# Optimization experiments

Hardware: AMD Instinct MI355X
Metric: run time of the kernel (lower is better)

The kernel has to match this reference:

```python
import jax, jax.numpy as jnp
import numpy as np

EMBED = 1024  # point_net_embedding_dim
H1, H2 = 512, 256  # head_hidden_layer_sizes


def _init(key, shape, fan_in):
    return jax.random.normal(key, shape, dtype=jnp.float32) / jnp.sqrt(jnp.float32(fan_in))


def setup_inputs() -> dict:
    key = jax.random.key(0)
    ks = jax.random.split(key, 13)
    B, N = 256, 1024
    x = jax.random.normal(ks[0], (B, N, 3), dtype=jnp.float32)
    # PointNet shared per-point MLP: 3 -> 64 -> 128 -> EMBED (ReLU), max-pool over points
    W1 = _init(ks[1], (3, 64), 3);        b1 = jnp.zeros((64,), jnp.float32)
    W2 = _init(ks[2], (64, 128), 64);     b2 = jnp.zeros((128,), jnp.float32)
    W3 = _init(ks[3], (128, EMBED), 128); b3 = jnp.zeros((EMBED,), jnp.float32)
    # Head MLP: EMBED -> 512 -> 256 -> 9 (no final activation)
    Wh1 = _init(ks[4], (EMBED, H1), EMBED); bh1 = jnp.zeros((H1,), jnp.float32)
    Wh2 = _init(ks[5], (H1, H2), H1);       bh2 = jnp.zeros((H2,), jnp.float32)
    Wh3 = _init(ks[6], (H2, 9), H2);        bh3 = jnp.zeros((9,), jnp.float32)
    return {"x": x, "W1": W1, "b1": b1, "W2": W2, "b2": b2, "W3": W3, "b3": b3,
            "Wh1": Wh1, "bh1": bh1, "Wh2": Wh2, "bh2": bh2, "Wh3": Wh3, "bh3": bh3}


def svd_projection(M):
    # Project raw 3x3 matrices onto SO(3): R = U diag(1,1,det(U V^T)) V^T
    U, S, Vh = jnp.linalg.svd(M, full_matrices=False)
    det = jnp.linalg.det(jnp.einsum('...ij,...jk->...ik', U, Vh))
    d = jnp.stack([jnp.ones_like(det), jnp.ones_like(det), det], axis=-1)  # [..., 3]
    return jnp.einsum('...ij,...j,...jk->...ik', U, d, Vh)


def reference(x, W1, b1, W2, b2, W3, b3, Wh1, bh1, Wh2, bh2, Wh3, bh3):
    # Shared per-point MLP (ReLU), final_activation=ReLU, then max-pool over points
    h = jax.nn.relu(x @ W1 + b1)          # [B, N, 64]
    h = jax.nn.relu(h @ W2 + b2)          # [B, N, 128]
    h = jax.nn.relu(h @ W3 + b3)          # [B, N, EMBED]
    g = jnp.max(h, axis=-2)               # [B, EMBED] global feature
    # Head MLP -> raw 3x3
    z = jax.nn.relu(g @ Wh1 + bh1)
    z = jax.nn.relu(z @ Wh2 + bh2)
    raw = (z @ Wh3 + bh3).reshape(*x.shape[:-2], 3, 3)
    return svd_projection(raw)
```

## Files before the change

### kernel.cpp

```cpp
#include <hip/hip_runtime.h>
#include <math.h>

typedef _Float16 f16;
typedef _Float16 f16x8 __attribute__((ext_vector_type(8)));
typedef float f32x4 __attribute__((ext_vector_type(4)));

__device__ __forceinline__ void glds16(const void* g, void* l) {
    __builtin_amdgcn_global_load_lds(
        (const __attribute__((address_space(1))) unsigned int*)g,
        (__attribute__((address_space(3))) unsigned int*)l, 16, 0, 0);
}

__global__ __launch_bounds__(256, 2) void pointnet_l12(
    const float* __restrict__ x,
    const float* __restrict__ W1, const float* __restrict__ b1,
    const float* __restrict__ W2, const float* __restrict__ b2,
    f16* __restrict__ h2)
{
    __shared__ float xs[512*3];
    __shared__ float w1s[192], b1s[64], b2s[128];
    __shared__ __align__(16) f16 h2s[128*136];

    int tid = threadIdx.x;
    int P0 = blockIdx.x * 512;
    for (int i = tid; i < 1536; i += 256) xs[i] = x[(size_t)P0*3 + i];
    if (tid < 192) w1s[tid] = W1[tid];
    else b1s[tid - 192] = b1[tid - 192];
    if (tid < 128) b2s[tid] = b2[tid];

    int lane = tid & 63, wid = tid >> 6;
    int wr = wid & 1, wc = wid >> 1;
    int lrow = lane & 15, quad = lane >> 4;

    f16x8 bf[4][2];
#pragma unroll
    for (int ct = 0; ct < 4; ct++)
#pragma unroll
        for (int kc = 0; kc < 2; kc++) {
            int col = wc*64 + ct*16 + lrow;
#pragma unroll
            for (int j = 0; j < 8; j++)
                bf[ct][kc][j] = (f16)W2[(size_t)(kc*32 + quad*8 + j)*128 + col];
        }

    __syncthreads();

    for (int mt = 0; mt < 4; mt++) {
        f32x4 acc[4][4];
#pragma unroll
        for (int rt = 0; rt < 4; rt++)
#pragma unroll
            for (int ct = 0; ct < 4; ct++)
                acc[rt][ct] = (f32x4){0.f, 0.f, 0.f, 0.f};

#pragma unroll
        for (int kc = 0; kc < 2; kc++) {
            float wa[8], wb[8], wcv[8], bv[8];
#pragma unroll
            for (int j = 0; j < 8; j++) {
                int k = kc*32 + quad*8 + j;
                wa[j] = w1s[k]; wb[j] = w1s[64+k]; wcv[j] = w1s[128+k]; bv[j] = b1s[k];
            }
            f16x8 af[4];
#pragma unroll
            for (int rt = 0; rt < 4; rt++) {
                int p = mt*128 + wr*64 + rt*16 + lrow;
                float x0 = xs[p*3], x1 = xs[p*3+1], x2 = xs[p*3+2];
#pragma unroll
                for (int j = 0; j < 8; j++) {
                    float v = fmaf(x2, wcv[j], fmaf(x1, wb[j], fmaf(x0, wa[j], bv[j])));
                    af[rt][j] = (f16)fmaxf(v, 0.f);
                }
            }
#pragma unroll
            for (int rt = 0; rt < 4; rt++)
#pragma unroll
                for (int ct = 0; ct < 4; ct++)
                    acc[rt][ct] = __builtin_amdgcn_mfma_f32_16x16x32_f16(af[rt], bf[ct][kc], acc[rt][ct], 0, 0, 0);
        }

        __syncthreads();
#pragma unroll
        for (int rt = 0; rt < 4; rt++)
#pragma unroll
            for (int ct = 0; ct < 4; ct++) {
                int col  = wc*64 + ct*16 + lrow;
                float bb = b2s[col];
                int rowb = wr*64 + rt*16 + quad*4;
#pragma unroll
                for (int r = 0; r < 4; r++) {
                    float v = fmaxf(acc[rt][ct][r] + bb, 0.f);
                    h2s[(rowb + r)*136 + col] = (f16)v;
                }
            }
        __syncthreads();
        size_t gbase = ((size_t)P0 + (size_t)mt*128) * 128;
#pragma unroll
        for (int i = 0; i < 8; i++) {
            int e = i*256 + tid;
            int row = e >> 4, c = e & 15;
            f16x8 v = *(const f16x8*)(h2s + row*136 + c*8);
            *(f16x8*)(h2 + gbase + (size_t)row*128 + ((c ^ (row & 15)) * 8)) = v;
        }
    }
}

__global__ __launch_bounds__(256, 2) void pointnet_l3_max(
    const f16* __restrict__ h2,
    const float* __restrict__ W3,
    const float* __restrict__ b3,
    float* __restrict__ g)
{
    __shared__ __align__(16) f16 atile[2][128 * 128];

    int i  = blockIdx.x;
    int b  = i & 255, nb = i >> 8;
    int tid = threadIdx.x;
    int lane = tid & 63, wid = tid >> 6;
    int lrow = lane & 15, quad = lane >> 4;
    int col0 = nb*256 + wid*64;

    f16x8 bf[4][4];
#pragma unroll
    for (int ct = 0; ct < 4; ct++)
#pragma unroll
        for (int kc = 0; kc < 4; kc++) {
            int col = col0 + ct*16 + lrow;
#pragma unroll
            for (int j = 0; j < 8; j++)
                bf[ct][kc][j] = (f16)W3[(size_t)(kc*32 + quad*8 + j)*1024 + col];
        }

    float cmax[4] = {-3.0e38f, -3.0e38f, -3.0e38f, -3.0e38f};
    const f16* abase = h2 + (size_t)b * 1024 * 128;

    {
        const f16* gsrc = abase;
#pragma unroll
        for (int s = 0; s < 8; s++)
            glds16(gsrc + (wid*512 + s*64 + lane)*8, atile[0] + (wid*512 + s*64)*8);
    }

    int cur = 0;
    for (int m0 = 0; m0 < 1024; m0 += 128) {
        __syncthreads();
        if (m0 + 128 < 1024) {
            const f16* gsrc = abase + (size_t)(m0 + 128) * 128;
            f16* ldst = atile[cur ^ 1];
#pragma unroll
            for (int s = 0; s < 8; s++)
                glds16(gsrc + (wid*512 + s*64 + lane)*8, ldst + (wid*512 + s*64)*8);
        }

        const f16* at = atile[cur];
#pragma unroll
        for (int half = 0; half < 2; half++) {
            f32x4 acc[4][4];
#pragma unroll
            for (int rt = 0; rt < 4; rt++)
#pragma unroll
                for (int ct = 0; ct < 4; ct++)
                    acc[rt][ct] = (f32x4){0.f, 0.f, 0.f, 0.f};
#pragma unroll
            for (int kc = 0; kc < 4; kc++) {
                f16x8 af[4];
#pragma unroll
                for (int rt = 0; rt < 4; rt++) {
                    int row  = half*64 + rt*16 + lrow;
                    int slot = (kc*4 + quad) ^ lrow;
                    af[rt] = *(const f16x8*)(at + row*128 + slot*8);
                }
#pragma unroll
                for (int rt = 0; rt < 4; rt++)
#pragma unroll
                    for (int ct = 0; ct < 4; ct++)
                        acc[rt][ct] = __builtin_amdgcn_mfma_f32_16x16x32_f16(af[rt], bf[ct][kc], acc[rt][ct], 0, 0, 0);
            }
#pragma unroll
            for (int rt = 0; rt < 4; rt++)
#pragma unroll
                for (int ct = 0; ct < 4; ct++)
#pragma unroll
                    for (int r = 0; r < 4; r++)
                        cmax[ct] = fmaxf(cmax[ct], acc[rt][ct][r]);
        }
        cur ^= 1;
    }

#pragma unroll
    for (int ct = 0; ct < 4; ct++) {
        cmax[ct] = fmaxf(cmax[ct], __shfl_xor(cmax[ct], 16, 64));
        cmax[ct] = fmaxf(cmax[ct], __shfl_xor(cmax[ct], 32, 64));
    }
    if (quad == 0) {
#pragma unroll
        for (int ct = 0; ct < 4; ct++) {
            int cg = col0 + ct*16 + lrow;
            g[(size_t)b*1024 + cg] = fmaxf(cmax[ct] + b3[cg], 0.f);
        }
    }
}

__global__ __launch_bounds__(256) void head_l1(
    const float* __restrict__ g, const float* __restrict__ Wh1,
    float* __restrict__ zp1)
{
    __shared__ float gs4[4][256];
    int cb = blockIdx.x, bb = blockIdx.y, kc = blockIdx.z;
    int tid = threadIdx.x;
    int b0 = bb * 4;
    int kbase = kc * 256;
#pragma unroll
    for (int j = 0; j < 4; j++) {
        int i = tid + j*256;
        gs4[i >> 8][i & 255] = g[(size_t)(b0 + (i >> 8))*1024 + kbase + (i & 255)];
    }
    __syncthreads();

    int c = cb*256 + tid;
    float acc[4] = {0.f, 0.f, 0.f, 0.f};
#pragma unroll 1
    for (int k = 0; k < 256; k += 8) {
        float w[8];
#pragma unroll
        for (int j = 0; j < 8; j++) w[j] = Wh1[(size_t)(kbase+k+j)*512 + c];
#pragma unroll
        for (int r = 0; r < 4; r++) {
            float4 a = *(const float4*)&gs4[r][k];
            float4 bq = *(const float4*)&gs4[r][k+4];
            acc[r] = fmaf(a.x, w[0], acc[r]);
            acc[r] = fmaf(a.y, w[1], acc[r]);
            acc[r] = fmaf(a.z, w[2], acc[r]);
            acc[r] = fmaf(a.w, w[3], acc[r]);
            acc[r] = fmaf(bq.x, w[4], acc[r]);
            acc[r] = fmaf(bq.y, w[5], acc[r]);
            acc[r] = fmaf(bq.z, w[6], acc[r]);
            acc[r] = fmaf(bq.w, w[7], acc[r]);
        }
    }
#pragma unroll
    for (int r = 0; r < 4; r++)
        zp1[((size_t)kc*256 + b0 + r)*512 + c] = acc[r];
}

__global__ __launch_bounds__(256) void head_l2(
    const float* __restrict__ zp1, const float* __restrict__ bh1,
    const float* __restrict__ Wh2, float* __restrict__ zp2)
{
    __shared__ float z1s[2][128];
    int bb = blockIdx.x, kc2 = blockIdx.y;
    int tid = threadIdx.x;
    int b0 = bb * 2;
    int kb = kc2 * 128;
    {
        int row = tid >> 7, kk = tid & 127;
        int col = kb + kk;
        float v = bh1[col];
#pragma unroll
        for (int j = 0; j < 4; j++)
            v += zp1[((size_t)j*256 + b0 + row)*512 + col];
        z1s[row][kk] = fmaxf(v, 0.f);
    }
    __syncthreads();

    int c = tid;
    float acc0 = 0.f, acc1 = 0.f;
#pragma unroll 1
    for (int k = 0; k < 128; k += 8) {
        float w[8];
#pragma unroll
        for (int j = 0; j < 8; j++) w[j] = Wh2[(size_t)(kb+k+j)*256 + c];
        float4 a0 = *(const float4*)&z1s[0][k];
        float4 a1 = *(const float4*)&z1s[0][k+4];
        float4 d0 = *(const float4*)&z1s[1][k];
        float4 d1 = *(const float4*)&z1s[1][k+4];
        acc0 = fmaf(a0.x, w[0], acc0);  acc1 = fmaf(d0.x, w[0], acc1);
        acc0 = fmaf(a0.y, w[1], acc0);  acc1 = fmaf(d0.y, w[1], acc1);
        acc0 = fmaf(a0.z, w[2], acc0);  acc1 = fmaf(d0.z, w[2], acc1);
        acc0 = fmaf(a0.w, w[3], acc0);  acc1 = fmaf(d0.w, w[3], acc1);
        acc0 = fmaf(a1.x, w[4], acc0);  acc1 = fmaf(d1.x, w[4], acc1);
        acc0 = fmaf(a1.y, w[5], acc0);  acc1 = fmaf(d1.y, w[5], acc1);
        acc0 = fmaf(a1.z, w[6], acc0);  acc1 = fmaf(d1.z, w[6], acc1);
        acc0 = fmaf(a1.w, w[7], acc0);  acc1 = fmaf(d1.w, w[7], acc1);
    }
    zp2[((size_t)kc2*256 + b0    )*256 + c] = acc0;
    zp2[((size_t)kc2*256 + b0 + 1)*256 + c] = acc1;
}

__device__ inline void jrot(double S[3][3], double V[3][3], int p, int q)
{
    double apq = S[p][q];
    if (fabs(apq) < 1e-36) return;
    double tau = (S[q][q] - S[p][p]) / (2.0 * apq);
    double t = (tau >= 0.0 ? 1.0 : -1.0) / (fabs(tau) + sqrt(1.0 + tau*tau));
    double c = 1.0 / sqrt(1.0 + t*t);
    double s = t * c;
    for (int k = 0; k < 3; k++) {
        double skp = S[k][p], skq = S[k][q];
        S[k][p] = c*skp - s*skq;  S[k][q] = s*skp + c*skq;
    }
    for (int k = 0; k < 3; k++) {
        double spk = S[p][k], sqk = S[q][k];
        S[p][k] = c*spk - s*sqk;  S[q][k] = s*spk + c*sqk;
    }
    for (int k = 0; k < 3; k++) {
        double vkp = V[k][p], vkq = V[k][q];
        V[k][p] = c*vkp - s*vkq;  V[k][q] = s*vkp + c*vkq;
    }
}

__device__ void svd_so3(const float* Mf, float* Rout)
{
    double M[3][3], S[3][3], V[3][3];
    for (int i = 0; i < 3; i++)
        for (int j = 0; j < 3; j++) M[i][j] = (double)Mf[3*i+j];
    for (int i = 0; i < 3; i++)
        for (int j = 0; j < 3; j++)
            S[i][j] = M[0][i]*M[0][j] + M[1][i]*M[1][j] + M[2][i]*M[2][j];
    for (int i = 0; i < 3; i++)
        for (int j = 0; j < 3; j++) V[i][j] = (i == j) ? 1.0 : 0.0;
    for (int it = 0; it < 10; it++) {
        jrot(S, V, 0, 1); jrot(S, V, 0, 2); jrot(S, V, 1, 2);
    }
    double lam[3] = {S[0][0], S[1][1], S[2][2]};
    int i0 = 0, i1 = 1, i2 = 2, tt;
    if (lam[i0] < lam[i1]) { tt = i0; i0 = i1; i1 = tt; }
    if (lam[i0] < lam[i2]) { tt = i0; i0 = i2; i2 = tt; }
    if (lam[i1] < lam[i2]) { tt = i1; i1 = i2; i2 = tt; }
    double v0[3], v1[3], v2[3];
    for (int k = 0; k < 3; k++) { v0[k] = V[k][i0]; v1[k] = V[k][i1]; v2[k] = V[k][i2]; }
    double u1[3], u2[3], u3[3];
    for (int i = 0; i < 3; i++) u1[i] = M[i][0]*v0[0] + M[i][1]*v0[1] + M[i][2]*v0[2];
    double n1 = sqrt(u1[0]*u1[0] + u1[1]*u1[1] + u1[2]*u1[2]) + 1e-300;
    for (int i = 0; i < 3; i++) u1[i] /= n1;
    for (int i = 0; i < 3; i++) u2[i] = M[i][0]*v1[0] + M[i][1]*v1[1] + M[i][2]*v1[2];
    double d12 = u1[0]*u2[0] + u1[1]*u2[1] + u1[2]*u2[2];
    for (int i = 0; i < 3; i++) u2[i] -= d12*u1[i];
    double n2 = sqrt(u2[0]*u2[0] + u2[1]*u2[1] + u2[2]*u2[2]) + 1e-300;
    for (int i = 0; i < 3; i++) u2[i] /= n2;
    u3[0] = u1[1]*u2[2] - u1[2]*u2[1];
    u3[1] = u1[2]*u2[0] - u1[0]*u2[2];
    u3[2] = u1[0]*u2[1] - u1[1]*u2[0];
    double c12x = v1[1]*v2[2] - v1[2]*v2[1];
    double c12y = v1[2]*v2[0] - v1[0]*v2[2];
    double c12z = v1[0]*v2[1] - v1[1]*v2[0];
    double detV = v0[0]*c12x + v0[1]*c12y + v0[2]*c12z;
    for (int i = 0; i < 3; i++)
        for (int j = 0; j < 3; j++)
            Rout[3*i+j] = (float)(u1[i]*v0[j] + u2[i]*v1[j] + detV*u3[i]*v2[j]);
}

__global__ __launch_bounds__(128) void head_l3_svd(
    const float* __restrict__ zp2, const float* __restrict__ bh2,
    const float* __restrict__ Wh3, const float* __restrict__ bh3,
    float* __restrict__ out)
{
    __shared__ float z2s[8][256];
    __shared__ float wh3s[2304];
    __shared__ float raws[8][12];
    int b0 = blockIdx.x * 8;
    int tid = threadIdx.x;

    for (int i = tid; i < 2304; i += 128) wh3s[i] = Wh3[i];
    for (int i = tid; i < 8*256; i += 128) {
        int row = i >> 8, kk = i & 255;
        float v = bh2[kk];
#pragma unroll
        for (int j = 0; j < 4; j++)
            v += zp2[((size_t)j*256 + b0 + row)*256 + kk];
        z2s[row][kk] = fmaxf(v, 0.f);
    }
    __syncthreads();

    if (tid < 72) {
        int r = tid / 9, c = tid % 9;
        float acc = bh3[c];
#pragma unroll 8
        for (int k = 0; k < 256; k++) acc = fmaf(z2s[r][k], wh3s[k*9 + c], acc);
        raws[r][c] = acc;
    }
    __syncthreads();

    if (tid < 8) svd_so3(&raws[tid][0], out + (size_t)(b0 + tid)*9);
}

extern "C" void kernel_launch(void* const* d_in, const int* in_sizes, int n_in,
                              void* d_out, int out_size, void* d_ws, size_t ws_size,
                              hipStream_t stream)
{
    const float* x   = (const float*)d_in[0];
    const float* W1  = (const float*)d_in[1];
    const float* b1  = (const float*)d_in[2];
    const float* W2  = (const float*)d_in[3];
    const float* b2  = (const float*)d_in[4];
    const float* W3  = (const float*)d_in[5];
    const float* b3  = (const float*)d_in[6];
    const float* Wh1 = (const float*)d_in[7];
    const float* bh1 = (const float*)d_in[8];
    const float* Wh2 = (const float*)d_in[9];
    const float* bh2 = (const float*)d_in[10];
    const float* Wh3 = (const float*)d_in[11];
    const float* bh3 = (const float*)d_in[12];
    float* out = (float*)d_out;

    char* ws = (char*)d_ws;
    f16*   h2  = (f16*)ws;
    float* g   = (float*)(ws + (size_t)67108864);
    float* zp1 = (float*)(ws + (size_t)67108864 + 1048576);
    float* zp2 = (float*)(ws + (size_t)67108864 + 1048576 + 2097152);

    pointnet_l12<<<512, 256, 0, stream>>>(x, W1, b1, W2, b2, h2);
    pointnet_l3_max<<<1024, 256, 0, stream>>>(h2, W3, b3, g);
    dim3 gridH1(2, 64, 4);
    head_l1<<<gridH1, 256, 0, stream>>>(g, Wh1, zp1);
    dim3 gridH2(128, 4);
    head_l2<<<gridH2, 256, 0, stream>>>(zp1, bh1, Wh2, zp2);
    head_l3_svd<<<32, 128, 0, stream>>>(zp2, bh2, Wh3, bh3, out);
}
```

Baseline: 190.2 us.

## Fuse PointNet layers 1-3 and max-pool into one kernel, pretransposing weights

Merges the layer-1/2 kernel and the layer-3+max kernel into one kernel per batch item, so the 64 MB f16 h2 intermediate never goes to global memory. Layer-2 output goes into a double-buffered LDS tile and feeds layer-3 MFMAs, with layer-2 of the next chunk overlapped with layer-3 of the current one. A new prep kernel transposes and casts W2/W3 to f16 and packs W1/b1, so per-thread fragments load as vectors. The cost is only 256 blocks of 512 threads with heavy register use (32 f16x8 B fragments for W3), which limits occupancy, plus an extra launch.

```diff
diff --git a/kernel.cpp b/kernel.cpp
--- a/kernel.cpp
+++ b/kernel.cpp
@@ -5,198 +5,163 @@
 typedef _Float16 f16x8 __attribute__((ext_vector_type(8)));
 typedef float f32x4 __attribute__((ext_vector_type(4)));
 
-__device__ __forceinline__ void glds16(const void* g, void* l) {
-    __builtin_amdgcn_global_load_lds(
-        (const __attribute__((address_space(1))) unsigned int*)g,
-        (__attribute__((address_space(3))) unsigned int*)l, 16, 0, 0);
-}
-
-__global__ __launch_bounds__(256, 2) void pointnet_l12(
+__global__ __launch_bounds__(256) void prep_weights(
+    const float* __restrict__ W1, const float* __restrict__ b1,
+    const float* __restrict__ W2, const float* __restrict__ W3,
+    f16* __restrict__ W2t, f16* __restrict__ W3t, float* __restrict__ wpk)
+{
+    int idx = blockIdx.x * 256 + threadIdx.x;
+    int stride = gridDim.x * 256;
+    for (int i = idx; i < 1024 * 128; i += stride) {
+        int c = i >> 7, k = i & 127;
+        W3t[i] = (f16)W3[k * 1024 + c];
+    }
+    for (int i = idx; i < 128 * 64; i += stride) {
+        int c = i >> 6, k = i & 63;
+        W2t[i] = (f16)W2[k * 128 + c];
+    }
+    if (idx < 256) {
+        int k = idx >> 2, c = idx & 3;
+        wpk[idx] = (c < 3) ? W1[c * 64 + k] : b1[k];
+    }
+}
+
+__global__ __launch_bounds__(512, 2) void pointnet_fused(
     const float* __restrict__ x,
-    const float* __restrict__ W1, const float* __restrict__ b1,
-    const float* __restrict__ W2, const float* __restrict__ b2,
-    f16* __restrict__ h2)
-{
-    __shared__ float xs[512*3];
-    __shared__ float w1s[192], b1s[64], b2s[128];
-    __shared__ __align__(16) f16 h2s[128*136];
-
-    int tid = threadIdx.x;
-    int P0 = blockIdx.x * 512;
-    for (int i = tid; i < 1536; i += 256) xs[i] = x[(size_t)P0*3 + i];
-    if (tid < 192) w1s[tid] = W1[tid];
-    else b1s[tid - 192] = b1[tid - 192];
-    if (tid < 128) b2s[tid] = b2[tid];
-
-    int lane = tid & 63, wid = tid >> 6;
-    int wr = wid & 1, wc = wid >> 1;
-    int lrow = lane & 15, quad = lane >> 4;
-
-    f16x8 bf[4][2];
-#pragma unroll
-    for (int ct = 0; ct < 4; ct++)
-#pragma unroll
-        for (int kc = 0; kc < 2; kc++) {
-            int col = wc*64 + ct*16 + lrow;
-#pragma unroll
-            for (int j = 0; j < 8; j++)
-                bf[ct][kc][j] = (f16)W2[(size_t)(kc*32 + quad*8 + j)*128 + col];
-        }
-
-    __syncthreads();
-
-    for (int mt = 0; mt < 4; mt++) {
-        f32x4 acc[4][4];
-#pragma unroll
-        for (int rt = 0; rt < 4; rt++)
-#pragma unroll
-            for (int ct = 0; ct < 4; ct++)
-                acc[rt][ct] = (f32x4){0.f, 0.f, 0.f, 0.f};
-
-#pragma unroll
-        for (int kc = 0; kc < 2; kc++) {
-            float wa[8], wb[8], wcv[8], bv[8];
-#pragma unroll
-            for (int j = 0; j < 8; j++) {
-                int k = kc*32 + quad*8 + j;
-                wa[j] = w1s[k]; wb[j] = w1s[64+k]; wcv[j] = w1s[128+k]; bv[j] = b1s[k];
-            }
-            f16x8 af[4];
-#pragma unroll
-            for (int rt = 0; rt < 4; rt++) {
-                int p = mt*128 + wr*64 + rt*16 + lrow;
-                float x0 = xs[p*3], x1 = xs[p*3+1], x2 = xs[p*3+2];
-#pragma unroll
-                for (int j = 0; j < 8; j++) {
-                    float v = fmaf(x2, wcv[j], fmaf(x1, wb[j], fmaf(x0, wa[j], bv[j])));
-                    af[rt][j] = (f16)fmaxf(v, 0.f);
-                }
-            }
-#pragma unroll
-            for (int rt = 0; rt < 4; rt++)
-#pragma unroll
-                for (int ct = 0; ct < 4; ct++)
-                    acc[rt][ct] = __builtin_amdgcn_mfma_f32_16x16x32_f16(af[rt], bf[ct][kc], acc[rt][ct], 0, 0, 0);
-        }
-
-        __syncthreads();
-#pragma unroll
-        for (int rt = 0; rt < 4; rt++)
-#pragma unroll
-            for (int ct = 0; ct < 4; ct++) {
-                int col  = wc*64 + ct*16 + lrow;
-                float bb = b2s[col];
-                int rowb = wr*64 + rt*16 + quad*4;
-#pragma unroll
-                for (int r = 0; r < 4; r++) {
-                    float v = fmaxf(acc[rt][ct][r] + bb, 0.f);
-                    h2s[(rowb + r)*136 + col] = (f16)v;
-                }
-            }
-        __syncthreads();
-        size_t gbase = ((size_t)P0 + (size_t)mt*128) * 128;
-#pragma unroll
-        for (int i = 0; i < 8; i++) {
-            int e = i*256 + tid;
-            int row = e >> 4, c = e & 15;
-            f16x8 v = *(const f16x8*)(h2s + row*136 + c*8);
-            *(f16x8*)(h2 + gbase + (size_t)row*128 + ((c ^ (row & 15)) * 8)) = v;
-        }
-    }
-}
-
-__global__ __launch_bounds__(256, 2) void pointnet_l3_max(
-    const f16* __restrict__ h2,
-    const float* __restrict__ W3,
+    const float* __restrict__ wpk,
+    const f16* __restrict__ W2t,
+    const float* __restrict__ b2,
+    const f16* __restrict__ W3t,
     const float* __restrict__ b3,
     float* __restrict__ g)
 {
-    __shared__ __align__(16) f16 atile[2][128 * 128];
-
-    int i  = blockIdx.x;
-    int b  = i & 255, nb = i >> 8;
+    __shared__ float xs[1024 * 3];
+    __shared__ __align__(16) float wls[288];
+    __shared__ float b2s[128];
+    __shared__ __align__(16) f16 h2s[2][128 * 136];
+
+    int b = blockIdx.x;
     int tid = threadIdx.x;
-    int lane = tid & 63, wid = tid >> 6;
+    int lane = tid & 63, w = tid >> 6;
     int lrow = lane & 15, quad = lane >> 4;
-    int col0 = nb*256 + wid*64;
-
-    f16x8 bf[4][4];
-#pragma unroll
-    for (int ct = 0; ct < 4; ct++)
-#pragma unroll
-        for (int kc = 0; kc < 4; kc++) {
-            int col = col0 + ct*16 + lrow;
-#pragma unroll
-            for (int j = 0; j < 8; j++)
-                bf[ct][kc][j] = (f16)W3[(size_t)(kc*32 + quad*8 + j)*1024 + col];
-        }
-
-    float cmax[4] = {-3.0e38f, -3.0e38f, -3.0e38f, -3.0e38f};
-    const f16* abase = h2 + (size_t)b * 1024 * 128;
-
+    int wr2 = w & 3, wc2 = w >> 2;
+
+    f16x8 bf3[8][4];
     {
-        const f16* gsrc = abase;
-#pragma unroll
-        for (int s = 0; s < 8; s++)
-            glds16(gsrc + (wid*512 + s*64 + lane)*8, atile[0] + (wid*512 + s*64)*8);
-    }
-
-    int cur = 0;
-    for (int m0 = 0; m0 < 1024; m0 += 128) {
+        const f16* base = W3t + (size_t)(w * 128 + lrow) * 128 + quad * 8;
+#pragma unroll
+        for (int ct = 0; ct < 8; ct++)
+#pragma unroll
+            for (int kc = 0; kc < 4; kc++)
+                bf3[ct][kc] = *(const f16x8*)(base + ct * 16 * 128 + kc * 32);
+    }
+    f16x8 bf2[4][2];
+    {
+        const f16* base = W2t + (size_t)(wc2 * 64 + lrow) * 64 + quad * 8;
+#pragma unroll
+        for (int ct = 0; ct < 4; ct++)
+#pragma unroll
+            for (int kc2 = 0; kc2 < 2; kc2++)
+                bf2[ct][kc2] = *(const f16x8*)(base + ct * 16 * 64 + kc2 * 32);
+    }
+
+    {
+        const float* xb = x + (size_t)b * 3072;
+        for (int i = tid; i < 3072; i += 512) xs[i] = xb[i];
+        if (tid < 256) {
+            int k = tid >> 2, c = tid & 3;
+            wls[(k + (k >> 3)) * 4 + c] = wpk[tid];
+        }
+        if (tid >= 256 && tid < 384) b2s[tid - 256] = b2[tid - 256];
+    }
+    __syncthreads();
+
+    const f32x4 z4 = {0.f, 0.f, 0.f, 0.f};
+    float cmax[8];
+#pragma unroll
+    for (int ct = 0; ct < 8; ct++) cmax[ct] = -3.0e38f;
+
+    auto phaseA = [&](int chunk) {
+        f16* hb = h2s[chunk & 1];
+        int p0 = chunk * 128 + wr2 * 32 + lrow;
+        float x00 = xs[p0 * 3], x01 = xs[p0 * 3 + 1], x02 = xs[p0 * 3 + 2];
+        int p1 = p0 + 16;
+        float x10 = xs[p1 * 3], x11 = xs[p1 * 3 + 1], x12 = xs[p1 * 3 + 2];
+        f32x4 acc2[2][4];
+#pragma unroll
+        for (int kc2 = 0; kc2 < 2; kc2++) {
+            f16x8 af2[2];
+#pragma unroll
+            for (int j = 0; j < 8; j++) {
+                int k = kc2 * 32 + quad * 8 + j;
+                f32x4 wv = *(const f32x4*)&wls[(k + (k >> 3)) * 4];
+                float v0 = fmaf(x02, wv[2], fmaf(x01, wv[1], fmaf(x00, wv[0], wv[3])));
+                float v1 = fmaf(x12, wv[2], fmaf(x11, wv[1], fmaf(x10, wv[0], wv[3])));
+                af2[0][j] = (f16)fmaxf(v0, 0.f);
+                af2[1][j] = (f16)fmaxf(v1, 0.f);
+            }
+#pragma unroll
+            for (int rt = 0; rt < 2; rt++)
+#pragma unroll
+                for (int ct = 0; ct < 4; ct++)
+                    acc2[rt][ct] = __builtin_amdgcn_mfma_f32_16x16x32_f16(
+                        af2[rt], bf2[ct][kc2], kc2 ? acc2[rt][ct] : z4, 0, 0, 0);
+        }
+#pragma unroll
+        for (int rt = 0; rt < 2; rt++)
+#pragma unroll
+            for (int ct = 0; ct < 4; ct++) {
+                int col = wc2 * 64 + ct * 16 + lrow;
+                float bb = b2s[col];
+                int rowb = wr2 * 32 + rt * 16 + quad * 4;
+#pragma unroll
+                for (int r = 0; r < 4; r++)
+                    hb[(rowb + r) * 136 + col] = (f16)fmaxf(acc2[rt][ct][r] + bb, 0.f);
+            }
+    };
+
+    auto phaseB = [&](int chunk) {
+        const f16* hb = h2s[chunk & 1];
+#pragma unroll
+        for (int rt = 0; rt < 8; rt++) {
+            f32x4 acc[8];
+#pragma unroll
+            for (int kc = 0; kc < 4; kc++) {
+                f16x8 af = *(const f16x8*)(hb + (rt * 16 + lrow) * 136 + kc * 32 + quad * 8);
+#pragma unroll
+                for (int ct = 0; ct < 8; ct++)
+                    acc[ct] = __builtin_amdgcn_mfma_f32_16x16x32_f16(
+                        af, bf3[ct][kc], kc ? acc[ct] : z4, 0, 0, 0);
+            }
+#pragma unroll
+            for (int ct = 0; ct < 8; ct++) {
+                float m01 = fmaxf(acc[ct][0], acc[ct][1]);
+                float m23 = fmaxf(acc[ct][2], acc[ct][3]);
+                cmax[ct] = fmaxf(cmax[ct], fmaxf(m01, m23));
+            }
+        }
+    };
+
+    phaseA(0);
+    __syncthreads();
+#pragma unroll 1
+    for (int c = 0; c < 7; c++) {
+        phaseA(c + 1);
+        phaseB(c);
         __syncthreads();
-        if (m0 + 128 < 1024) {
-            const f16* gsrc = abase + (size_t)(m0 + 128) * 128;
-            f16* ldst = atile[cur ^ 1];
-#pragma unroll
-            for (int s = 0; s < 8; s++)
-                glds16(gsrc + (wid*512 + s*64 + lane)*8, ldst + (wid*512 + s*64)*8);
-        }
-
-        const f16* at = atile[cur];
-#pragma unroll
-        for (int half = 0; half < 2; half++) {
-            f32x4 acc[4][4];
-#pragma unroll
-            for (int rt = 0; rt < 4; rt++)
-#pragma unroll
-                for (int ct = 0; ct < 4; ct++)
-                    acc[rt][ct] = (f32x4){0.f, 0.f, 0.f, 0.f};
-#pragma unroll
-            for (int kc = 0; kc < 4; kc++) {
-                f16x8 af[4];
-#pragma unroll
-                for (int rt = 0; rt < 4; rt++) {
-                    int row  = half*64 + rt*16 + lrow;
-                    int slot = (kc*4 + quad) ^ lrow;
-                    af[rt] = *(const f16x8*)(at + row*128 + slot*8);
-                }
-#pragma unroll
-                for (int rt = 0; rt < 4; rt++)
-#pragma unroll
-                    for (int ct = 0; ct < 4; ct++)
-                        acc[rt][ct] = __builtin_amdgcn_mfma_f32_16x16x32_f16(af[rt], bf[ct][kc], acc[rt][ct], 0, 0, 0);
-            }
-#pragma unroll
-            for (int rt = 0; rt < 4; rt++)
-#pragma unroll
-                for (int ct = 0; ct < 4; ct++)
-#pragma unroll
-                    for (int r = 0; r < 4; r++)
-                        cmax[ct] = fmaxf(cmax[ct], acc[rt][ct][r]);
-        }
-        cur ^= 1;
-    }
-
-#pragma unroll
-    for (int ct = 0; ct < 4; ct++) {
+    }
+    phaseB(7);
+
+#pragma unroll
+    for (int ct = 0; ct < 8; ct++) {
         cmax[ct] = fmaxf(cmax[ct], __shfl_xor(cmax[ct], 16, 64));
         cmax[ct] = fmaxf(cmax[ct], __shfl_xor(cmax[ct], 32, 64));
     }
     if (quad == 0) {
 #pragma unroll
-        for (int ct = 0; ct < 4; ct++) {
-            int cg = col0 + ct*16 + lrow;
-            g[(size_t)b*1024 + cg] = fmaxf(cmax[ct] + b3[cg], 0.f);
+        for (int ct = 0; ct < 8; ct++) {
+            int cg = w * 128 + ct * 16 + lrow;
+            g[(size_t)b * 1024 + cg] = fmaxf(cmax[ct] + b3[cg], 0.f);
         }
     }
 }
@@ -212,22 +177,22 @@
     int kbase = kc * 256;
 #pragma unroll
     for (int j = 0; j < 4; j++) {
-        int i = tid + j*256;
-        gs4[i >> 8][i & 255] = g[(size_t)(b0 + (i >> 8))*1024 + kbase + (i & 255)];
-    }
-    __syncthreads();
-
-    int c = cb*256 + tid;
+        int i = tid + j * 256;
+        gs4[i >> 8][i & 255] = g[(size_t)(b0 + (i >> 8)) * 1024 + kbase + (i & 255)];
+    }
+    __syncthreads();
+
+    int c = cb * 256 + tid;
     float acc[4] = {0.f, 0.f, 0.f, 0.f};
 #pragma unroll 1
     for (int k = 0; k < 256; k += 8) {
         float w[8];
 #pragma unroll
-        for (int j = 0; j < 8; j++) w[j] = Wh1[(size_t)(kbase+k+j)*512 + c];
+        for (int j = 0; j < 8; j++) w[j] = Wh1[(size_t)(kbase + k + j) * 512 + c];
 #pragma unroll
         for (int r = 0; r < 4; r++) {
             float4 a = *(const float4*)&gs4[r][k];
-            float4 bq = *(const float4*)&gs4[r][k+4];
+            float4 bq = *(const float4*)&gs4[r][k + 4];
             acc[r] = fmaf(a.x, w[0], acc[r]);
             acc[r] = fmaf(a.y, w[1], acc[r]);
             acc[r] = fmaf(a.z, w[2], acc[r]);
@@ -240,7 +205,7 @@
     }
 #pragma unroll
     for (int r = 0; r < 4; r++)
-        zp1[((size_t)kc*256 + b0 + r)*512 + c] = acc[r];
+        zp1[((size_t)kc * 256 + b0 + r) * 512 + c] = acc[r];
 }
 
 __global__ __launch_bounds__(256) void head_l2(
@@ -258,7 +223,7 @@
         float v = bh1[col];
 #pragma unroll
         for (int j = 0; j < 4; j++)
-            v += zp1[((size_t)j*256 + b0 + row)*512 + col];
+            v += zp1[((size_t)j * 256 + b0 + row) * 512 + col];
         z1s[row][kk] = fmaxf(v, 0.f);
     }
     __syncthreads();
@@ -269,11 +234,11 @@
     for (int k = 0; k < 128; k += 8) {
         float w[8];
 #pragma unroll
-        for (int j = 0; j < 8; j++) w[j] = Wh2[(size_t)(kb+k+j)*256 + c];
+        for (int j = 0; j < 8; j++) w[j] = Wh2[(size_t)(kb + k + j) * 256 + c];
         float4 a0 = *(const float4*)&z1s[0][k];
-        float4 a1 = *(const float4*)&z1s[0][k+4];
+        float4 a1 = *(const float4*)&z1s[0][k + 4];
         float4 d0 = *(const float4*)&z1s[1][k];
-        float4 d1 = *(const float4*)&z1s[1][k+4];
+        float4 d1 = *(const float4*)&z1s[1][k + 4];
         acc0 = fmaf(a0.x, w[0], acc0);  acc1 = fmaf(d0.x, w[0], acc1);
         acc0 = fmaf(a0.y, w[1], acc0);  acc1 = fmaf(d0.y, w[1], acc1);
         acc0 = fmaf(a0.z, w[2], acc0);  acc1 = fmaf(d0.z, w[2], acc1);
@@ -283,8 +248,8 @@
         acc0 = fmaf(a1.z, w[6], acc0);  acc1 = fmaf(d1.z, w[6], acc1);
         acc0 = fmaf(a1.w, w[7], acc0);  acc1 = fmaf(d1.w, w[7], acc1);
     }
-    zp2[((size_t)kc2*256 + b0    )*256 + c] = acc0;
-    zp2[((size_t)kc2*256 + b0 + 1)*256 + c] = acc1;
+    zp2[((size_t)kc2 * 256 + b0    ) * 256 + c] = acc0;
+    zp2[((size_t)kc2 * 256 + b0 + 1) * 256 + c] = acc1;
 }
 
 __device__ inline void jrot(double S[3][3], double V[3][3], int p, int q)
@@ -292,20 +257,20 @@
     double apq = S[p][q];
     if (fabs(apq) < 1e-36) return;
     double tau = (S[q][q] - S[p][p]) / (2.0 * apq);
-    double t = (tau >= 0.0 ? 1.0 : -1.0) / (fabs(tau) + sqrt(1.0 + tau*tau));
-    double c = 1.0 / sqrt(1.0 + t*t);
+    double t = (tau >= 0.0 ? 1.0 : -1.0) / (fabs(tau) + sqrt(1.0 + tau * tau));
+    double c = 1.0 / sqrt(1.0 + t * t);
     double s = t * c;
     for (int k = 0; k < 3; k++) {
         double skp = S[k][p], skq = S[k][q];
-        S[k][p] = c*skp - s*skq;  S[k][q] = s*skp + c*skq;
+        S[k][p] = c * skp - s * skq;  S[k][q] = s * skp + c * skq;
     }
     for (int k = 0; k < 3; k++) {
         double spk = S[p][k], sqk = S[q][k];
-        S[p][k] = c*spk - s*sqk;  S[q][k] = s*spk + c*sqk;
+        S[p][k] = c * spk - s * sqk;  S[q][k] = s * spk + c * sqk;
     }
     for (int k = 0; k < 3; k++) {
         double vkp = V[k][p], vkq = V[k][q];
-        V[k][p] = c*vkp - s*vkq;  V[k][q] = s*vkp + c*vkq;
+        V[k][p] = c * vkp - s * vkq;  V[k][q] = s * vkp + c * vkq;
     }
 }
 
@@ -313,10 +278,10 @@
 {
     double M[3][3], S[3][3], V[3][3];
     for (int i = 0; i < 3; i++)
-        for (int j = 0; j < 3; j++) M[i][j] = (double)Mf[3*i+j];
+        for (int j = 0; j < 3; j++) M[i][j] = (double)Mf[3 * i + j];
     for (int i = 0; i < 3; i++)
         for (int j = 0; j < 3; j++)
-            S[i][j] = M[0][i]*M[0][j] + M[1][i]*M[1][j] + M[2][i]*M[2][j];
+            S[i][j] = M[0][i] * M[0][j] + M[1][i] * M[1][j] + M[2][i] * M[2][j];
     for (int i = 0; i < 3; i++)
         for (int j = 0; j < 3; j++) V[i][j] = (i == j) ? 1.0 : 0.0;
     for (int it = 0; it < 10; it++) {
@@ -330,24 +295,24 @@
     double v0[3], v1[3], v2[3];
     for (int k = 0; k < 3; k++) { v0[k] = V[k][i0]; v1[k] = V[k][i1]; v2[k] = V[k][i2]; }
     double u1[3], u2[3], u3[3];
-    for (int i = 0; i < 3; i++) u1[i] = M[i][0]*v0[0] + M[i][1]*v0[1] + M[i][2]*v0[2];
-    double n1 = sqrt(u1[0]*u1[0] + u1[1]*u1[1] + u1[2]*u1[2]) + 1e-300;
+    for (int i = 0; i < 3; i++) u1[i] = M[i][0] * v0[0] + M[i][1] * v0[1] + M[i][2] * v0[2];
+    double n1 = sqrt(u1[0] * u1[0] + u1[1] * u1[1] + u1[2] * u1[2]) + 1e-300;
     for (int i = 0; i < 3; i++) u1[i] /= n1;
-    for (int i = 0; i < 3; i++) u2[i] = M[i][0]*v1[0] + M[i][1]*v1[1] + M[i][2]*v1[2];
-    double d12 = u1[0]*u2[0] + u1[1]*u2[1] + u1[2]*u2[2];
-    for (int i = 0; i < 3; i++) u2[i] -= d12*u1[i];
-    double n2 = sqrt(u2[0]*u2[0] + u2[1]*u2[1] + u2[2]*u2[2]) + 1e-300;
+    for (int i = 0; i < 3; i++) u2[i] = M[i][0] * v1[0] + M[i][1] * v1[1] + M[i][2] * v1[2];
+    double d12 = u1[0] * u2[0] + u1[1] * u2[1] + u1[2] * u2[2];
+    for (int i = 0; i < 3; i++) u2[i] -= d12 * u1[i];
+    double n2 = sqrt(u2[0] * u2[0] + u2[1] * u2[1] + u2[2] * u2[2]) + 1e-300;
     for (int i = 0; i < 3; i++) u2[i] /= n2;
-    u3[0] = u1[1]*u2[2] - u1[2]*u2[1];
-    u3[1] = u1[2]*u2[0] - u1[0]*u2[2];
-    u3[2] = u1[0]*u2[1] - u1[1]*u2[0];
-    double c12x = v1[1]*v2[2] - v1[2]*v2[1];
-    double c12y = v1[2]*v2[0] - v1[0]*v2[2];
-    double c12z = v1[0]*v2[1] - v1[1]*v2[0];
-    double detV = v0[0]*c12x + v0[1]*c12y + v0[2]*c12z;
+    u3[0] = u1[1] * u2[2] - u1[2] * u2[1];
+    u3[1] = u1[2] * u2[0] - u1[0] * u2[2];
+    u3[2] = u1[0] * u2[1] - u1[1] * u2[0];
+    double c12x = v1[1] * v2[2] - v1[2] * v2[1];
+    double c12y = v1[2] * v2[0] - v1[0] * v2[2];
+    double c12z = v1[0] * v2[1] - v1[1] * v2[0];
+    double detV = v0[0] * c12x + v0[1] * c12y + v0[2] * c12z;
     for (int i = 0; i < 3; i++)
         for (int j = 0; j < 3; j++)
-            Rout[3*i+j] = (float)(u1[i]*v0[j] + u2[i]*v1[j] + detV*u3[i]*v2[j]);
+            Rout[3 * i + j] = (float)(u1[i] * v0[j] + u2[i] * v1[j] + detV * u3[i] * v2[j]);
 }
 
 __global__ __launch_bounds__(128) void head_l3_svd(
@@ -362,12 +327,12 @@
     int tid = threadIdx.x;
 
     for (int i = tid; i < 2304; i += 128) wh3s[i] = Wh3[i];
-    for (int i = tid; i < 8*256; i += 128) {
+    for (int i = tid; i < 8 * 256; i += 128) {
         int row = i >> 8, kk = i & 255;
         float v = bh2[kk];
 #pragma unroll
         for (int j = 0; j < 4; j++)
-            v += zp2[((size_t)j*256 + b0 + row)*256 + kk];
+            v += zp2[((size_t)j * 256 + b0 + row) * 256 + kk];
         z2s[row][kk] = fmaxf(v, 0.f);
     }
     __syncthreads();
@@ -376,12 +341,12 @@
         int r = tid / 9, c = tid % 9;
         float acc = bh3[c];
 #pragma unroll 8
-        for (int k = 0; k < 256; k++) acc = fmaf(z2s[r][k], wh3s[k*9 + c], acc);
+        for (int k = 0; k < 256; k++) acc = fmaf(z2s[r][k], wh3s[k * 9 + c], acc);
         raws[r][c] = acc;
     }
     __syncthreads();
 
-    if (tid < 8) svd_so3(&raws[tid][0], out + (size_t)(b0 + tid)*9);
+    if (tid < 8) svd_so3(&raws[tid][0], out + (size_t)(b0 + tid) * 9);
 }
 
 extern "C" void kernel_launch(void* const* d_in, const int* in_sizes, int n_in,
@@ -404,13 +369,15 @@
     float* out = (float*)d_out;
 
     char* ws = (char*)d_ws;
-    f16*   h2  = (f16*)ws;
-    float* g   = (float*)(ws + (size_t)67108864);
-    float* zp1 = (float*)(ws + (size_t)67108864 + 1048576);
-    float* zp2 = (float*)(ws + (size_t)67108864 + 1048576 + 2097152);
-
-    pointnet_l12<<<512, 256, 0, stream>>>(x, W1, b1, W2, b2, h2);
-    pointnet_l3_max<<<1024, 256, 0, stream>>>(h2, W3, b3, g);
+    f16*   W2t = (f16*)ws;
+    f16*   W3t = (f16*)(ws + 65536);
+    float* wpk = (float*)(ws + 524288);
+    float* g   = (float*)(ws + 1048576);
+    float* zp1 = (float*)(ws + 2097152);
+    float* zp2 = (float*)(ws + 4194304);
+
+    prep_weights<<<128, 256, 0, stream>>>(W1, b1, W2, W3, W2t, W3t, wpk);
+    pointnet_fused<<<256, 512, 0, stream>>>(x, wpk, W2t, b2, W3t, b3, g);
     dim3 gridH1(2, 64, 4);
     head_l1<<<gridH1, 256, 0, stream>>>(g, Wh1, zp1);
     dim3 gridH2(128, 4);
```

Result: faster. 177.6 us (-6.6%).
